# Optimization experiments

Hardware: AMD Instinct MI355X
Metric: run time of the kernel (lower is better)

## Reference

```python
import jax, jax.numpy as jnp
import numpy as np

P_SIZE = 5
NUM_HEAD = 8
GN_EPS = 1e-5
LRELU_SLOPE = 0.2


def conv1x1(w, x, b=None):
    # w: [out_c, in_c], x: [n, in_c, h, w]
    y = jnp.einsum('oc,nchw->nohw', w, x)
    if b is not None:
        y = y + b[None, :, None, None]
    return y


def bilinear_sample(feat, sx, sy):
    """grid_sample(mode='bilinear', padding_mode='zeros', align_corners=True).
    With align_corners=True the normalize/denormalize round-trip in
    deformation_grid/grid_sample is the identity, so sx,sy are raw pixel coords.
    feat: [n,c,H,W]; sx,sy: [n,P,H,W] -> out [n,c,P,H,W]."""
    n, c, H, W = feat.shape
    x0 = jnp.floor(sx)
    y0 = jnp.floor(sy)
    x1 = x0 + 1.0
    y1 = y0 + 1.0
    wx1 = sx - x0
    wx0 = 1.0 - wx1
    wy1 = sy - y0
    wy0 = 1.0 - wy1
    feat_flat = feat.reshape(n, c, H * W)

    def corner(xi, yi, wgt):
        valid = (xi >= 0) & (xi <= W - 1) & (yi >= 0) & (yi <= H - 1)
        xc = jnp.clip(xi, 0, W - 1).astype(jnp.int32)
        yc = jnp.clip(yi, 0, H - 1).astype(jnp.int32)
        idx = (yc * W + xc).reshape(n, -1)                      # [n, P*H*W]
        g = jnp.take_along_axis(feat_flat, idx[:, None, :], axis=2)  # [n,c,P*H*W]
        g = g.reshape(n, c, xi.shape[1], H, W)                  # [n,c,P,H,W]
        wm = (wgt * valid.astype(feat.dtype))[:, None]          # [n,1,P,H,W]
        return g * wm

    return (corner(x0, y0, wx0 * wy0) + corner(x1, y0, wx1 * wy0)
            + corner(x0, y1, wx0 * wy1) + corner(x1, y1, wx1 * wy1))


def sample_coords(deform_field, p_size):
    # deform_field: [n,2,h,w] -> absolute pixel coords sx, sy: [n, p^2, h, w]
    n, _, h, w = deform_field.shape
    padding = (p_size - 1) // 2
    shift = jnp.arange(p_size, dtype=deform_field.dtype) - padding
    shift_y, shift_x = jnp.meshgrid(shift, shift, indexing='ij')  # [p,p]
    shift_y = shift_y.reshape(-1, 1, 1)  # [p^2,1,1]
    shift_x = shift_x.reshape(-1, 1, 1)
    gy = jnp.arange(h, dtype=deform_field.dtype)[:, None]  # [h,1]
    gx = jnp.arange(w, dtype=deform_field.dtype)[None, :]  # [1,w]
    sx = gx[None] + shift_x + deform_field[:, None, 0]     # [n,p^2,h,w]
    sy = gy[None] + shift_y + deform_field[:, None, 1]
    return sx, sy


def setup_inputs() -> dict:
    key = jax.random.key(0)
    ks = jax.random.split(key, 12)
    n, c, h, w = 2, 128, 96, 96
    hid = 256
    s = 0.05
    return {
        'query': jax.random.normal(ks[0], (n, c, h, w), jnp.float32),
        'key': jax.random.normal(ks[1], (n, c, h, w), jnp.float32),
        'value': jax.random.normal(ks[2], (n, c, h, w), jnp.float32),
        'deform_field': jax.random.normal(ks[3], (n, 2, h, w), jnp.float32) * 2.0,
        'w_q': jax.random.normal(ks[4], (c, c), jnp.float32) * s,
        'w_k': jax.random.normal(ks[5], (c, c), jnp.float32) * s,
        'w_v': jax.random.normal(ks[6], (c, c), jnp.float32) * s,
        'w_fc': jax.random.normal(ks[7], (c, c), jnp.float32) * s,
        'mlp_w1': jax.random.normal(ks[8], (hid, c), jnp.float32) * s,
        'mlp_b1': jnp.zeros((hid,), jnp.float32),
        'mlp_w2': jax.random.normal(ks[9], (c, hid), jnp.float32) * s,
        'mlp_b2': jnp.zeros((c,), jnp.float32),
        'gn_gamma': jnp.ones((c,), jnp.float32),
        'gn_beta': jnp.zeros((c,), jnp.float32),
    }


def reference(query, key, value, deform_field, w_q, w_k, w_v, w_fc,
              mlp_w1, mlp_b1, mlp_w2, mlp_b2, gn_gamma, gn_beta):
    p2 = P_SIZE * P_SIZE
    n, c, h, w = query.shape
    d_k = c // NUM_HEAD

    q = conv1x1(w_q, query)   # [n,c,h,w]
    k = conv1x1(w_k, key)
    v = conv1x1(w_v, value)

    # deformable window sampling of keys/values
    sx, sy = sample_coords(deform_field, P_SIZE)      # [n,p^2,h,w]
    k_s = bilinear_sample(k, sx, sy)                  # [n,c,p^2,h,w]
    v_s = bilinear_sample(v, sx, sy)

    # split heads
    q = q.reshape(n, NUM_HEAD, d_k, h, w)
    k_s = k_s.reshape(n, NUM_HEAD, d_k, p2, h, w)
    v_s = v_s.reshape(n, NUM_HEAD, d_k, p2, h, w)

    scale = 1.0 / jnp.sqrt(jnp.asarray(d_k, q.dtype))
    attn = jnp.einsum('nedyx,nedpyx->neyxp', q * scale, k_s)   # [n,head,h,w,p^2]
    attn = jax.nn.softmax(attn, axis=-1)
    out = jnp.einsum('neyxp,nedpyx->nedyx', attn, v_s)          # [n,head,d_v,h,w]
    out = out.reshape(n, c, h, w)
    out = conv1x1(w_fc, out)

    # conv-MLP residual
    hdn = conv1x1(mlp_w1, out, mlp_b1)
    hdn = jnp.where(hdn >= 0, hdn, LRELU_SLOPE * hdn)
    out = out + conv1x1(mlp_w2, hdn, mlp_b2)

    # GroupNorm(1, feat_dim): normalize over (C,H,W) per sample, per-channel affine
    mean = jnp.mean(out, axis=(1, 2, 3), keepdims=True)
    var = jnp.mean(jnp.square(out - mean), axis=(1, 2, 3), keepdims=True)
    out = (out - mean) * jax.lax.rsqrt(var + GN_EPS)
    out = out * gn_gamma[None, :, None, None] + gn_beta[None, :, None, None]
    return out
```

## Files before the change

### kernel.cpp

```cpp
#include <hip/hip_runtime.h>
#include <cstddef>

constexpr int Cc = 128;
constexpr int Hh = 96;
constexpr int Ww = 96;
constexpr int HW = Hh * Ww;
constexpr int Nn = 2;

typedef __attribute__((ext_vector_type(2))) _Float16 f16x2;
typedef __attribute__((ext_vector_type(4))) _Float16 f16x4;
typedef __attribute__((ext_vector_type(8))) _Float16 f16x8;
typedef __attribute__((ext_vector_type(4))) float f32x4;

__device__ __forceinline__ float fdot2(f16x2 a, f16x2 b, float c) {
#if defined(__has_builtin) && __has_builtin(__builtin_amdgcn_fdot2)
    return __builtin_amdgcn_fdot2(a, b, c, false);
#else
    return (float)a[0] * (float)b[0] + (float)a[1] * (float)b[1] + c;
#endif
}

__global__ void __launch_bounds__(256)
wcvt_k(const float* __restrict__ wq, const float* __restrict__ wk,
       const float* __restrict__ wv, const float* __restrict__ wfc,
       const float* __restrict__ w1, const float* __restrict__ w2,
       _Float16* __restrict__ dst)
{
    const int h0 = (blockIdx.x * 256 + threadIdx.x) * 8;
    const float* src; int off, K;
    if (h0 < 16384)      { src = wq;  off = h0;          K = 128; }
    else if (h0 < 32768) { src = wk;  off = h0 - 16384;  K = 128; }
    else if (h0 < 49152) { src = wv;  off = h0 - 32768;  K = 128; }
    else if (h0 < 65536) { src = wfc; off = h0 - 49152;  K = 128; }
    else if (h0 < 98304) { src = w1;  off = h0 - 65536;  K = 128; }
    else                 { src = w2;  off = h0 - 98304;  K = 256; }
    const int fid  = off >> 3;
    const int lane = fid & 63;
    const int n16  = lane & 15, quad = lane >> 4;
    const int t2   = fid >> 6;
    const int kcN  = K / 32;
    const int kc   = t2 % kcN;
    const int mt   = t2 / kcN;
    const int row  = mt * 16 + n16;
    const int col  = kc * 32 + quad * 8;
    const float* s = src + (size_t)row * K + col;
    const float4 a = *(const float4*)s;
    const float4 b = *(const float4*)(s + 4);
    f16x8 h = {(_Float16)a.x, (_Float16)a.y, (_Float16)a.z, (_Float16)a.w,
               (_Float16)b.x, (_Float16)b.y, (_Float16)b.z, (_Float16)b.w};
    *(f16x8*)&dst[h0] = h;
}

__global__ void __launch_bounds__(128)
kv_k(const float* __restrict__ Xk, const float* __restrict__ Xv,
     const _Float16* __restrict__ w16,
     _Float16* __restrict__ k16, _Float16* __restrict__ v16)
{
    const int t  = blockIdx.y;
    const int p0 = blockIdx.x * 64;
    const int z  = blockIdx.z;
    const float* X = (t == 0) ? Xk : Xv;
    _Float16* Y    = (t == 0) ? k16 : v16;
    const _Float16* W = w16 + 16384 + (size_t)t * 16384;

    __shared__ _Float16 xl[128][72];
    const int tid = threadIdx.x;
    {
        const int px4 = (tid & 15) * 4, kg = tid >> 4;
        const float* Xz = X + (size_t)z * Cc * HW + p0 + px4;
#pragma unroll
        for (int kk = 0; kk < 16; ++kk) {
            const int k = kk * 8 + kg;
            float4 a = *(const float4*)&Xz[(size_t)k * HW];
            f16x4 h = {(_Float16)a.x, (_Float16)a.y, (_Float16)a.z, (_Float16)a.w};
            *(f16x4*)&xl[k][px4] = h;
        }
    }
    __syncthreads();

    const int w = tid >> 6, lane = tid & 63;
    const int n16 = lane & 15, quad = lane >> 4;
    const int pw = w * 32;

    f16x8 A[2][4];
#pragma unroll
    for (int mi = 0; mi < 2; ++mi) {
        const int px = pw + mi * 16 + n16;
#pragma unroll
        for (int kcid = 0; kcid < 4; ++kcid) {
            f16x8 av;
#pragma unroll
            for (int j = 0; j < 8; ++j) av[j] = xl[kcid * 32 + quad * 8 + j][px];
            A[mi][kcid] = av;
        }
    }

#pragma unroll
    for (int half = 0; half < 2; ++half) {
        const int oc0 = half * 64;
        f32x4 acc[2][4];
#pragma unroll
        for (int mi = 0; mi < 2; ++mi)
#pragma unroll
            for (int ni = 0; ni < 4; ++ni) acc[mi][ni] = (f32x4)0.f;

#pragma unroll
        for (int kcid = 0; kcid < 4; ++kcid) {
            f16x8 B[4];
#pragma unroll
            for (int ni = 0; ni < 4; ++ni)
                B[ni] = *(const f16x8*)&W[(((half * 4 + ni) * 4 + kcid) * 64 + lane) * 8];
#pragma unroll
            for (int mi = 0; mi < 2; ++mi)
#pragma unroll
                for (int ni = 0; ni < 4; ++ni)
                    acc[mi][ni] = __builtin_amdgcn_mfma_f32_16x16x32_f16(
                        A[mi][kcid], B[ni], acc[mi][ni], 0, 0, 0);
        }

#pragma unroll
        for (int mi = 0; mi < 2; ++mi)
#pragma unroll
            for (int r = 0; r < 4; ++r) {
                const int pix = p0 + pw + mi * 16 + quad * 4 + r;
                const size_t base = ((size_t)z * HW + pix) * Cc + oc0;
#pragma unroll
                for (int ni = 0; ni < 4; ++ni)
                    Y[base + ni * 16 + n16] = (_Float16)acc[mi][ni][r];
            }
    }
}

__global__ void __launch_bounds__(512)
qaf_k(const float* __restrict__ Xq, const _Float16* __restrict__ w16,
      const _Float16* __restrict__ k16, const _Float16* __restrict__ v16,
      const float* __restrict__ df, const float* __restrict__ b1,
      const float* __restrict__ b2, _Float16* __restrict__ y2,
      float* __restrict__ pb)
{
    __shared__ __align__(16) _Float16 xl[32][136];
    __shared__ __align__(16) _Float16 ql[32][136];
    __shared__ __align__(16) _Float16 y1l[32][136];
    __shared__ __align__(16) _Float16 hl[32][264];
    __shared__ float red[16];

    const int z  = blockIdx.z;
    const int bx = blockIdx.x;
    const int ti = (bx & 7) * 36 + (bx >> 3);
    const int p0 = ti * 32;
    const int tid = threadIdx.x, w = tid >> 6, lane = tid & 63;
    const int n16 = lane & 15, quad = lane >> 4;

    {
        const int px4 = (tid & 7) * 4, k0 = tid >> 3;
        const float* Xz = Xq + (size_t)z * Cc * HW + p0 + px4;
#pragma unroll
        for (int kk = 0; kk < 2; ++kk) {
            const int k = kk * 64 + k0;
            float4 a = *(const float4*)&Xz[(size_t)k * HW];
            xl[px4 + 0][k] = (_Float16)a.x;
            xl[px4 + 1][k] = (_Float16)a.y;
            xl[px4 + 2][k] = (_Float16)a.z;
            xl[px4 + 3][k] = (_Float16)a.w;
        }
    }
    __syncthreads();

    {
        f32x4 qa[2];
        qa[0] = (f32x4)0.f; qa[1] = (f32x4)0.f;
#pragma unroll
        for (int kc = 0; kc < 4; ++kc) {
            f16x8 A[2];
#pragma unroll
            for (int mi = 0; mi < 2; ++mi)
                A[mi] = *(const f16x8*)&xl[mi * 16 + n16][kc * 32 + quad * 8];
            const f16x8 B = *(const f16x8*)&w16[((w * 4 + kc) * 64 + lane) * 8];
#pragma unroll
            for (int mi = 0; mi < 2; ++mi)
                qa[mi] = __builtin_amdgcn_mfma_f32_16x16x32_f16(A[mi], B, qa[mi], 0, 0, 0);
        }
#pragma unroll
        for (int mi = 0; mi < 2; ++mi)
#pragma unroll
            for (int r = 0; r < 4; ++r)
                ql[mi * 16 + quad * 4 + r][w * 16 + n16] = (_Float16)qa[mi][r];
    }
    __syncthreads();

    {
        const int lpx = w * 4 + (lane >> 4);
        const int pix = p0 + lpx;
        const int y = pix / Ww, x = pix - y * Ww;
        const int co = n16 * 8;

        const float dx = df[((size_t)z * 2 + 0) * HW + pix];
        const float dy = df[((size_t)z * 2 + 1) * HW + pix];
        const float flx = floorf(dx), fly = floorf(dy);
        const int bxp = x - 2 + (int)flx;
        const int byp = y - 2 + (int)fly;
        const float wx1 = dx - flx, wx0 = 1.f - wx1;
        const float wy1 = dy - fly, wy0 = 1.f - wy1;
        const float s00 = wy0 * wx0 * 0.25f, s01 = wy0 * wx1 * 0.25f,
                    s10 = wy1 * wx0 * 0.25f, s11 = wy1 * wx1 * 0.25f;

        const f16x8 qv8 = *(const f16x8*)&ql[lpx][co];
        const f16x2 q0 = {qv8[0], qv8[1]}, q1 = {qv8[2], qv8[3]},
                    q2 = {qv8[4], qv8[5]}, q3 = {qv8[6], qv8[7]};

        const _Float16* kp = k16 + ((size_t)z * HW) * Cc + co;
        const _Float16* vp = v16 + ((size_t)z * HW) * Cc + co;

        const bool inb = (bxp >= 0) & (byp >= 0) & (bxp <= Ww - 6) & (byp <= Hh - 6);
        const int allin = __all(inb);

        float qk[36];
        if (allin) {
            const _Float16* kr = kp + (size_t)(byp * Ww + bxp) * Cc;
#pragma unroll
            for (int r = 0; r < 6; ++r) {
#pragma unroll
                for (int c = 0; c < 6; ++c) {
                    const f16x8 kv = *(const f16x8*)&kr[c * Cc];
                    f16x2 k0 = {kv[0], kv[1]}, k1 = {kv[2], kv[3]};
                    f16x2 k2 = {kv[4], kv[5]}, k3 = {kv[6], kv[7]};
                    float d = fdot2(q0, k0, 0.f);
                    d = fdot2(q1, k1, d);
                    d = fdot2(q2, k2, d);
                    d = fdot2(q3, k3, d);
                    qk[r * 6 + c] = d;
                }
                kr += Ww * Cc;
            }
        } else {
#pragma unroll
            for (int r = 0; r < 6; ++r) {
                const int yr = byp + r;
                const bool rv = (yr >= 0) & (yr < Hh);
                const int yc = min(max(yr, 0), Hh - 1);
                const _Float16* kr = kp + (size_t)(yc * Ww) * Cc;
#pragma unroll
                for (int c = 0; c < 6; ++c) {
                    const int xc = bxp + c;
                    const bool cv = rv & (xc >= 0) & (xc < Ww);
                    const int xcc = min(max(xc, 0), Ww - 1);
                    const f16x8 kv = *(const f16x8*)&kr[xcc * Cc];
                    f16x2 k0 = {kv[0], kv[1]}, k1 = {kv[2], kv[3]};
                    f16x2 k2 = {kv[4], kv[5]}, k3 = {kv[6], kv[7]};
                    float d = fdot2(q0, k0, 0.f);
                    d = fdot2(q1, k1, d);
                    d = fdot2(q2, k2, d);
                    d = fdot2(q3, k3, d);
                    qk[r * 6 + c] = cv ? d : 0.f;
                }
            }
        }

        float a[25];
#pragma unroll
        for (int py = 0; py < 5; ++py)
#pragma unroll
            for (int px = 0; px < 5; ++px) {
                float tv = s00 * qk[py * 6 + px];
                tv = fmaf(s01, qk[py * 6 + px + 1], tv);
                tv = fmaf(s10, qk[(py + 1) * 6 + px], tv);
                tv = fmaf(s11, qk[(py + 1) * 6 + px + 1], tv);
                a[py * 5 + px] = tv;
            }
#pragma unroll
        for (int i = 0; i < 25; ++i) a[i] += __shfl_xor(a[i], 1, 64);

        float mx = a[0];
#pragma unroll
        for (int i = 1; i < 25; ++i) mx = fmaxf(mx, a[i]);
        float ssum = 0.f;
#pragma unroll
        for (int i = 0; i < 25; ++i) { a[i] = __expf(a[i] - mx); ssum += a[i]; }
        const float inv = 1.f / ssum;

        float tmp[6][5];
#pragma unroll
        for (int r = 0; r < 6; ++r)
#pragma unroll
            for (int px = 0; px < 5; ++px) {
                float tv = 0.f;
                if (r < 5)  tv = a[r * 5 + px] * wy0;
                if (r >= 1) tv = fmaf(a[(r - 1) * 5 + px], wy1, tv);
                tmp[r][px] = tv;
            }
        float wsum[36];
#pragma unroll
        for (int r = 0; r < 6; ++r)
#pragma unroll
            for (int c = 0; c < 6; ++c) {
                float tv = 0.f;
                if (c < 5)  tv = tmp[r][c] * wx0;
                if (c >= 1) tv = fmaf(tmp[r][c - 1], wx1, tv);
                wsum[r * 6 + c] = tv;
            }

        float o[8] = {0.f, 0.f, 0.f, 0.f, 0.f, 0.f, 0.f, 0.f};
        if (allin) {
            const _Float16* vr = vp + (size_t)(byp * Ww + bxp) * Cc;
#pragma unroll
            for (int r = 0; r < 6; ++r) {
#pragma unroll
                for (int c = 0; c < 6; ++c) {
                    const f16x8 vv = *(const f16x8*)&vr[c * Cc];
                    const float wgt = wsum[r * 6 + c];
#pragma unroll
                    for (int j = 0; j < 8; ++j)
                        o[j] = fmaf(wgt, (float)vv[j], o[j]);
                }
                vr += Ww * Cc;
            }
        } else {
#pragma unroll
            for (int r = 0; r < 6; ++r) {
                const int yr = byp + r;
                const bool rv = (yr >= 0) & (yr < Hh);
                const int yc = min(max(yr, 0), Hh - 1);
                const _Float16* vr = vp + (size_t)(yc * Ww) * Cc;
#pragma unroll
                for (int c = 0; c < 6; ++c) {
                    const int xc = bxp + c;
                    const bool cv = rv & (xc >= 0) & (xc < Ww);
                    const int xcc = min(max(xc, 0), Ww - 1);
                    const f16x8 vv = *(const f16x8*)&vr[xcc * Cc];
                    const float wgt = cv ? wsum[r * 6 + c] : 0.f;
#pragma unroll
                    for (int j = 0; j < 8; ++j)
                        o[j] = fmaf(wgt, (float)vv[j], o[j]);
                }
            }
        }

        f16x8 ov;
#pragma unroll
        for (int j = 0; j < 8; ++j) ov[j] = (_Float16)(o[j] * inv);
        *(f16x8*)&ql[lpx][co] = ov;
    }
    __syncthreads();

    const _Float16* Wfc = w16 + 49152;
    const _Float16* W1  = w16 + 65536;
    const _Float16* W2  = w16 + 98304;

    f32x4 acc1[2];
    acc1[0] = (f32x4)0.f; acc1[1] = (f32x4)0.f;
#pragma unroll
    for (int kc = 0; kc < 4; ++kc) {
        f16x8 A[2];
#pragma unroll
        for (int mi = 0; mi < 2; ++mi)
            A[mi] = *(const f16x8*)&ql[mi * 16 + n16][kc * 32 + quad * 8];
        const f16x8 B = *(const f16x8*)&Wfc[((w * 4 + kc) * 64 + lane) * 8];
#pragma unroll
        for (int mi = 0; mi < 2; ++mi)
            acc1[mi] = __builtin_amdgcn_mfma_f32_16x16x32_f16(A[mi], B, acc1[mi], 0, 0, 0);
    }
#pragma unroll
    for (int mi = 0; mi < 2; ++mi)
#pragma unroll
        for (int r = 0; r < 4; ++r)
            y1l[mi * 16 + quad * 4 + r][w * 16 + n16] = (_Float16)acc1[mi][r];
    __syncthreads();

    {
        f32x4 acc2[2][2];
#pragma unroll
        for (int mi = 0; mi < 2; ++mi)
#pragma unroll
            for (int ni = 0; ni < 2; ++ni) acc2[mi][ni] = (f32x4)0.f;
#pragma unroll
        for (int kc = 0; kc < 4; ++kc) {
            f16x8 A[2];
#pragma unroll
            for (int mi = 0; mi < 2; ++mi)
                A[mi] = *(const f16x8*)&y1l[mi * 16 + n16][kc * 32 + quad * 8];
#pragma unroll
            for (int ni = 0; ni < 2; ++ni) {
                const f16x8 B = *(const f16x8*)&W1[(((w * 2 + ni) * 4 + kc) * 64 + lane) * 8];
#pragma unroll
                for (int mi = 0; mi < 2; ++mi)
                    acc2[mi][ni] = __builtin_amdgcn_mfma_f32_16x16x32_f16(
                        A[mi], B, acc2[mi][ni], 0, 0, 0);
            }
        }
        float b1v[2];
#pragma unroll
        for (int ni = 0; ni < 2; ++ni) b1v[ni] = b1[w * 32 + ni * 16 + n16];
#pragma unroll
        for (int mi = 0; mi < 2; ++mi)
#pragma unroll
            for (int ni = 0; ni < 2; ++ni)
#pragma unroll
                for (int r = 0; r < 4; ++r) {
                    float tv = acc2[mi][ni][r] + b1v[ni];
                    tv = tv >= 0.f ? tv : 0.2f * tv;
                    hl[mi * 16 + quad * 4 + r][w * 32 + ni * 16 + n16] = (_Float16)tv;
                }
    }
    __syncthreads();

    f32x4 acc3[2];
    acc3[0] = (f32x4)0.f; acc3[1] = (f32x4)0.f;
#pragma unroll
    for (int kc = 0; kc < 8; ++kc) {
        f16x8 A[2];
#pragma unroll
        for (int mi = 0; mi < 2; ++mi)
            A[mi] = *(const f16x8*)&hl[mi * 16 + n16][kc * 32 + quad * 8];
        const f16x8 B = *(const f16x8*)&W2[((w * 8 + kc) * 64 + lane) * 8];
#pragma unroll
        for (int mi = 0; mi < 2; ++mi)
            acc3[mi] = __builtin_amdgcn_mfma_f32_16x16x32_f16(A[mi], B, acc3[mi], 0, 0, 0);
    }

    const float b2v = b2[w * 16 + n16];
    float lsum = 0.f, lsq = 0.f;
#pragma unroll
    for (int mi = 0; mi < 2; ++mi)
#pragma unroll
        for (int r = 0; r < 4; ++r) {
            const int pix = p0 + mi * 16 + quad * 4 + r;
            const float tv = acc3[mi][r] + b2v + acc1[mi][r];
            lsum += tv; lsq += tv * tv;
            y2[((size_t)z * HW + pix) * Cc + w * 16 + n16] = (_Float16)tv;
        }

#pragma unroll
    for (int m = 1; m < 64; m <<= 1) {
        lsum += __shfl_xor(lsum, m, 64);
        lsq  += __shfl_xor(lsq,  m, 64);
    }
    if (lane == 0) { red[w * 2] = lsum; red[w * 2 + 1] = lsq; }
    __syncthreads();
    if (tid == 0) {
        float S = 0.f, Q = 0.f;
#pragma unroll
        for (int i = 0; i < 8; ++i) { S += red[i * 2]; Q += red[i * 2 + 1]; }
        const int bid = z * (HW / 32) + bx;
        pb[bid * 2 + 0] = S;
        pb[bid * 2 + 1] = Q;
    }
}

__global__ void __launch_bounds__(256)
gn_k(const _Float16* __restrict__ y2, const float* __restrict__ pb,
     const float* __restrict__ gamma, const float* __restrict__ beta,
     float* __restrict__ out, const int nPerZ)
{
    __shared__ float t[32][68];
    __shared__ float redm[8];
    __shared__ float stats[2];
    const int z = blockIdx.z, c0 = blockIdx.y * 32, p0 = blockIdx.x * 64;
    const int tid = threadIdx.x;

    {
        float s = 0.f, qq = 0.f;
        for (int p = tid; p < nPerZ; p += 256) {
            s  += pb[(z * nPerZ + p) * 2 + 0];
            qq += pb[(z * nPerZ + p) * 2 + 1];
        }
#pragma unroll
        for (int m = 1; m < 64; m <<= 1) {
            s  += __shfl_xor(s,  m, 64);
            qq += __shfl_xor(qq, m, 64);
        }
        if ((tid & 63) == 0) {
            redm[(tid >> 6) * 2]     = s;
            redm[(tid >> 6) * 2 + 1] = qq;
        }
    }
    {
        const int px = tid >> 2, cq = tid & 3;
        const f16x8 a = *(const f16x8*)&y2[((size_t)z * HW + p0 + px) * Cc + c0 + cq * 8];
#pragma unroll
        for (int j = 0; j < 8; ++j) t[cq * 8 + j][px] = (float)a[j];
    }
    __syncthreads();
    if (tid == 0) {
        const float invN = 1.f / (float)(Cc * HW);
        const float S = redm[0] + redm[2] + redm[4] + redm[6];
        const float Q = redm[1] + redm[3] + redm[5] + redm[7];
        const float mean = S * invN;
        const float var  = fmaf(-mean, mean, Q * invN);
        stats[0] = mean;
        stats[1] = rsqrtf(var + 1e-5f);
    }
    __syncthreads();
    {
        const float mean = stats[0], rs = stats[1];
        const int c = tid >> 3, pq = tid & 7;
        const float g = gamma[c0 + c] * rs, be = beta[c0 + c];
        float4 o1, o2;
        o1.x = fmaf(t[c][pq * 8 + 0] - mean, g, be);
        o1.y = fmaf(t[c][pq * 8 + 1] - mean, g, be);
        o1.z = fmaf(t[c][pq * 8 + 2] - mean, g, be);
        o1.w = fmaf(t[c][pq * 8 + 3] - mean, g, be);
        o2.x = fmaf(t[c][pq * 8 + 4] - mean, g, be);
        o2.y = fmaf(t[c][pq * 8 + 5] - mean, g, be);
        o2.z = fmaf(t[c][pq * 8 + 6] - mean, g, be);
        o2.w = fmaf(t[c][pq * 8 + 7] - mean, g, be);
        float* dst = &out[((size_t)z * Cc + c0 + c) * HW + p0 + pq * 8];
        *(float4*)dst = o1;
        *(float4*)(dst + 4) = o2;
    }
}

extern "C" void kernel_launch(void* const* d_in, const int* in_sizes, int n_in,
                              void* d_out, int out_size, void* d_ws, size_t ws_size,
                              hipStream_t stream)
{
    const float* query  = (const float*)d_in[0];
    const float* key    = (const float*)d_in[1];
    const float* value  = (const float*)d_in[2];
    const float* deform = (const float*)d_in[3];
    const float* w_q    = (const float*)d_in[4];
    const float* w_k    = (const float*)d_in[5];
    const float* w_v    = (const float*)d_in[6];
    const float* w_fc   = (const float*)d_in[7];
    const float* mlp_w1 = (const float*)d_in[8];
    const float* mlp_b1 = (const float*)d_in[9];
    const float* mlp_w2 = (const float*)d_in[10];
    const float* mlp_b2 = (const float*)d_in[11];
    const float* gn_g   = (const float*)d_in[12];
    const float* gn_b   = (const float*)d_in[13];
    float* out = (float*)d_out;

    char* wsb = (char*)d_ws;
    _Float16* w16 = (_Float16*)wsb;
    float* pb   = (float*)(wsb + 262144);
    _Float16* T = (_Float16*)(wsb + 524288);
    const size_t S16 = (size_t)Nn * HW * Cc;
    _Float16* k16  = T;
    _Float16* v16  = T + S16;
    _Float16* y2h  = T + 2 * S16;

    wcvt_k<<<dim3(64), dim3(256), 0, stream>>>(
        w_q, w_k, w_v, w_fc, mlp_w1, mlp_w2, w16);

    kv_k<<<dim3(HW / 64, 2, Nn), dim3(128), 0, stream>>>(
        key, value, w16, k16, v16);

    qaf_k<<<dim3(HW / 32, 1, Nn), dim3(512), 0, stream>>>(
        query, w16, k16, v16, deform, mlp_b1, mlp_b2, y2h, pb);

    gn_k<<<dim3(HW / 64, Cc / 32, Nn), dim3(256), 0, stream>>>(
        y2h, pb, gn_g, gn_b, out, HW / 32);
}
```

Baseline: 146.1 us.

## Halve the fused attention kernel's pixel tile to 16 with 256-thread blocks

The fused query/attention/MLP kernel now processes 16 pixels per block with 4 waves instead of 32 pixels with 8 waves, which doubles the grid. Each wave now computes 32 output channels over the 16-pixel M tile rather than 16 channels over 32 pixels. The query input staging buffer is transposed to channel-major with packed half2 stores, and the MFMA A operand is gathered element by element. The intent is better CU load balance and occupancy with a smaller LDS footprint, in exchange for reading each weight tile for fewer pixels and for slower strided LDS gathers on the A operand. The partial-statistics count passed to the GroupNorm kernel is updated to match.

Measured after the change: 141.7 us. 3.0% less time.

```diff
diff --git a/kernel.cpp b/kernel.cpp
--- a/kernel.cpp
+++ b/kernel.cpp
@@ -131,37 +131,37 @@
     }
 }
 
-__global__ void __launch_bounds__(512)
+__global__ void __launch_bounds__(256)
 qaf_k(const float* __restrict__ Xq, const _Float16* __restrict__ w16,
       const _Float16* __restrict__ k16, const _Float16* __restrict__ v16,
       const float* __restrict__ df, const float* __restrict__ b1,
       const float* __restrict__ b2, _Float16* __restrict__ y2,
       float* __restrict__ pb)
 {
-    __shared__ __align__(16) _Float16 xl[32][136];
-    __shared__ __align__(16) _Float16 ql[32][136];
-    __shared__ __align__(16) _Float16 y1l[32][136];
-    __shared__ __align__(16) _Float16 hl[32][264];
-    __shared__ float red[16];
+    __shared__ __align__(16) _Float16 xl[128][18];
+    __shared__ __align__(16) _Float16 ql[16][140];
+    __shared__ __align__(16) _Float16 y1l[16][140];
+    __shared__ __align__(16) _Float16 hl[16][264];
+    __shared__ float red[8];
 
     const int z  = blockIdx.z;
     const int bx = blockIdx.x;
-    const int ti = (bx & 7) * 36 + (bx >> 3);
-    const int p0 = ti * 32;
+    const int ti = (bx & 7) * 72 + (bx >> 3);
+    const int p0 = ti * 16;
     const int tid = threadIdx.x, w = tid >> 6, lane = tid & 63;
     const int n16 = lane & 15, quad = lane >> 4;
 
     {
-        const int px4 = (tid & 7) * 4, k0 = tid >> 3;
+        const int px4 = (tid & 3) * 4, k0 = tid >> 2;
         const float* Xz = Xq + (size_t)z * Cc * HW + p0 + px4;
 #pragma unroll
         for (int kk = 0; kk < 2; ++kk) {
             const int k = kk * 64 + k0;
             float4 a = *(const float4*)&Xz[(size_t)k * HW];
-            xl[px4 + 0][k] = (_Float16)a.x;
-            xl[px4 + 1][k] = (_Float16)a.y;
-            xl[px4 + 2][k] = (_Float16)a.z;
-            xl[px4 + 3][k] = (_Float16)a.w;
+            f16x2 lo = {(_Float16)a.x, (_Float16)a.y};
+            f16x2 hi = {(_Float16)a.z, (_Float16)a.w};
+            *(f16x2*)&xl[k][px4]     = lo;
+            *(f16x2*)&xl[k][px4 + 2] = hi;
         }
     }
     __syncthreads();
@@ -171,20 +171,20 @@
         qa[0] = (f32x4)0.f; qa[1] = (f32x4)0.f;
 #pragma unroll
         for (int kc = 0; kc < 4; ++kc) {
-            f16x8 A[2];
-#pragma unroll
-            for (int mi = 0; mi < 2; ++mi)
-                A[mi] = *(const f16x8*)&xl[mi * 16 + n16][kc * 32 + quad * 8];
-            const f16x8 B = *(const f16x8*)&w16[((w * 4 + kc) * 64 + lane) * 8];
-#pragma unroll
-            for (int mi = 0; mi < 2; ++mi)
-                qa[mi] = __builtin_amdgcn_mfma_f32_16x16x32_f16(A[mi], B, qa[mi], 0, 0, 0);
-        }
-#pragma unroll
-        for (int mi = 0; mi < 2; ++mi)
+            f16x8 A;
+#pragma unroll
+            for (int j = 0; j < 8; ++j) A[j] = xl[kc * 32 + quad * 8 + j][n16];
+#pragma unroll
+            for (int ni = 0; ni < 2; ++ni) {
+                const f16x8 B = *(const f16x8*)&w16[(((w * 2 + ni) * 4 + kc) * 64 + lane) * 8];
+                qa[ni] = __builtin_amdgcn_mfma_f32_16x16x32_f16(A, B, qa[ni], 0, 0, 0);
+            }
+        }
+#pragma unroll
+        for (int ni = 0; ni < 2; ++ni)
 #pragma unroll
             for (int r = 0; r < 4; ++r)
-                ql[mi * 16 + quad * 4 + r][w * 16 + n16] = (_Float16)qa[mi][r];
+                ql[quad * 4 + r][w * 32 + ni * 16 + n16] = (_Float16)qa[ni][r];
     }
     __syncthreads();
 
@@ -350,56 +350,44 @@
     acc1[0] = (f32x4)0.f; acc1[1] = (f32x4)0.f;
 #pragma unroll
     for (int kc = 0; kc < 4; ++kc) {
-        f16x8 A[2];
-#pragma unroll
-        for (int mi = 0; mi < 2; ++mi)
-            A[mi] = *(const f16x8*)&ql[mi * 16 + n16][kc * 32 + quad * 8];
-        const f16x8 B = *(const f16x8*)&Wfc[((w * 4 + kc) * 64 + lane) * 8];
-#pragma unroll
-        for (int mi = 0; mi < 2; ++mi)
-            acc1[mi] = __builtin_amdgcn_mfma_f32_16x16x32_f16(A[mi], B, acc1[mi], 0, 0, 0);
-    }
-#pragma unroll
-    for (int mi = 0; mi < 2; ++mi)
+        const f16x8 A = *(const f16x8*)&ql[n16][kc * 32 + quad * 8];
+#pragma unroll
+        for (int ni = 0; ni < 2; ++ni) {
+            const f16x8 B = *(const f16x8*)&Wfc[(((w * 2 + ni) * 4 + kc) * 64 + lane) * 8];
+            acc1[ni] = __builtin_amdgcn_mfma_f32_16x16x32_f16(A, B, acc1[ni], 0, 0, 0);
+        }
+    }
+#pragma unroll
+    for (int ni = 0; ni < 2; ++ni)
 #pragma unroll
         for (int r = 0; r < 4; ++r)
-            y1l[mi * 16 + quad * 4 + r][w * 16 + n16] = (_Float16)acc1[mi][r];
-    __syncthreads();
-
-    {
-        f32x4 acc2[2][2];
-#pragma unroll
-        for (int mi = 0; mi < 2; ++mi)
-#pragma unroll
-            for (int ni = 0; ni < 2; ++ni) acc2[mi][ni] = (f32x4)0.f;
+            y1l[quad * 4 + r][w * 32 + ni * 16 + n16] = (_Float16)acc1[ni][r];
+    __syncthreads();
+
+    {
+        f32x4 acc2[4];
+#pragma unroll
+        for (int ni = 0; ni < 4; ++ni) acc2[ni] = (f32x4)0.f;
 #pragma unroll
         for (int kc = 0; kc < 4; ++kc) {
-            f16x8 A[2];
-#pragma unroll
-            for (int mi = 0; mi < 2; ++mi)
-                A[mi] = *(const f16x8*)&y1l[mi * 16 + n16][kc * 32 + quad * 8];
-#pragma unroll
-            for (int ni = 0; ni < 2; ++ni) {
-                const f16x8 B = *(const f16x8*)&W1[(((w * 2 + ni) * 4 + kc) * 64 + lane) * 8];
-#pragma unroll
-                for (int mi = 0; mi < 2; ++mi)
-                    acc2[mi][ni] = __builtin_amdgcn_mfma_f32_16x16x32_f16(
-                        A[mi], B, acc2[mi][ni], 0, 0, 0);
-            }
-        }
-        float b1v[2];
-#pragma unroll
-        for (int ni = 0; ni < 2; ++ni) b1v[ni] = b1[w * 32 + ni * 16 + n16];
-#pragma unroll
-        for (int mi = 0; mi < 2; ++mi)
-#pragma unroll
-            for (int ni = 0; ni < 2; ++ni)
-#pragma unroll
-                for (int r = 0; r < 4; ++r) {
-                    float tv = acc2[mi][ni][r] + b1v[ni];
-                    tv = tv >= 0.f ? tv : 0.2f * tv;
-                    hl[mi * 16 + quad * 4 + r][w * 32 + ni * 16 + n16] = (_Float16)tv;
-                }
+            const f16x8 A = *(const f16x8*)&y1l[n16][kc * 32 + quad * 8];
+#pragma unroll
+            for (int ni = 0; ni < 4; ++ni) {
+                const f16x8 B = *(const f16x8*)&W1[(((w * 4 + ni) * 4 + kc) * 64 + lane) * 8];
+                acc2[ni] = __builtin_amdgcn_mfma_f32_16x16x32_f16(A, B, acc2[ni], 0, 0, 0);
+            }
+        }
+        float b1v[4];
+#pragma unroll
+        for (int ni = 0; ni < 4; ++ni) b1v[ni] = b1[w * 64 + ni * 16 + n16];
+#pragma unroll
+        for (int ni = 0; ni < 4; ++ni)
+#pragma unroll
+            for (int r = 0; r < 4; ++r) {
+                float tv = acc2[ni][r] + b1v[ni];
+                tv = tv >= 0.f ? tv : 0.2f * tv;
+                hl[quad * 4 + r][w * 64 + ni * 16 + n16] = (_Float16)tv;
+            }
     }
     __syncthreads();
 
@@ -407,26 +395,27 @@
     acc3[0] = (f32x4)0.f; acc3[1] = (f32x4)0.f;
 #pragma unroll
     for (int kc = 0; kc < 8; ++kc) {
-        f16x8 A[2];
-#pragma unroll
-        for (int mi = 0; mi < 2; ++mi)
-            A[mi] = *(const f16x8*)&hl[mi * 16 + n16][kc * 32 + quad * 8];
-        const f16x8 B = *(const f16x8*)&W2[((w * 8 + kc) * 64 + lane) * 8];
-#pragma unroll
-        for (int mi = 0; mi < 2; ++mi)
-            acc3[mi] = __builtin_amdgcn_mfma_f32_16x16x32_f16(A[mi], B, acc3[mi], 0, 0, 0);
-    }
-
-    const float b2v = b2[w * 16 + n16];
+        const f16x8 A = *(const f16x8*)&hl[n16][kc * 32 + quad * 8];
+#pragma unroll
+        for (int ni = 0; ni < 2; ++ni) {
+            const f16x8 B = *(const f16x8*)&W2[(((w * 2 + ni) * 8 + kc) * 64 + lane) * 8];
+            acc3[ni] = __builtin_amdgcn_mfma_f32_16x16x32_f16(A, B, acc3[ni], 0, 0, 0);
+        }
+    }
+
+    float b2v[2];
+#pragma unroll
+    for (int ni = 0; ni < 2; ++ni) b2v[ni] = b2[w * 32 + ni * 16 + n16];
+
     float lsum = 0.f, lsq = 0.f;
 #pragma unroll
-    for (int mi = 0; mi < 2; ++mi)
+    for (int ni = 0; ni < 2; ++ni)
 #pragma unroll
         for (int r = 0; r < 4; ++r) {
-            const int pix = p0 + mi * 16 + quad * 4 + r;
-            const float tv = acc3[mi][r] + b2v + acc1[mi][r];
+            const int pix = p0 + quad * 4 + r;
+            const float tv = acc3[ni][r] + b2v[ni] + acc1[ni][r];
             lsum += tv; lsq += tv * tv;
-            y2[((size_t)z * HW + pix) * Cc + w * 16 + n16] = (_Float16)tv;
+            y2[((size_t)z * HW + pix) * Cc + w * 32 + ni * 16 + n16] = (_Float16)tv;
         }
 
 #pragma unroll
@@ -439,8 +428,8 @@
     if (tid == 0) {
         float S = 0.f, Q = 0.f;
 #pragma unroll
-        for (int i = 0; i < 8; ++i) { S += red[i * 2]; Q += red[i * 2 + 1]; }
-        const int bid = z * (HW / 32) + bx;
+        for (int i = 0; i < 4; ++i) { S += red[i * 2]; Q += red[i * 2 + 1]; }
+        const int bid = z * (HW / 16) + bx;
         pb[bid * 2 + 0] = S;
         pb[bid * 2 + 1] = Q;
     }
@@ -544,9 +533,9 @@
     kv_k<<<dim3(HW / 64, 2, Nn), dim3(128), 0, stream>>>(
         key, value, w16, k16, v16);
 
-    qaf_k<<<dim3(HW / 32, 1, Nn), dim3(512), 0, stream>>>(
+    qaf_k<<<dim3(HW / 16, 1, Nn), dim3(256), 0, stream>>>(
         query, w16, k16, v16, deform, mlp_b1, mlp_b2, y2h, pb);
 
     gn_k<<<dim3(HW / 64, Cc / 32, Nn), dim3(256), 0, stream>>>(
-        y2h, pb, gn_g, gn_b, out, HW / 32);
+        y2h, pb, gn_g, gn_b, out, HW / 16);
 }
```
